# Optimization experiments

Measured on AMD Instinct MI355X. Metric: run time of the kernel, lower is better.

## Reference

```python
import jax, jax.numpy as jnp
import numpy as np

FP8_E4M3_MAX = 448.0
FP4_E2M1_MAX = 6.0
BLOCK = 16  # NVFP4 block-scale granularity


def _round_e4m3(x):
    """Round non-negative values to fp8 e4m3 grid (3 mantissa bits, min normal 2^-6, max 448)."""
    a = jnp.abs(x)
    e = jnp.clip(jnp.floor(jnp.log2(jnp.where(a > 0, a, 1.0))), -6.0, 8.0)
    s = jnp.exp2(e)
    q = jnp.round(a / s * 8.0) / 8.0 * s
    q = jnp.clip(q, 0.0, FP8_E4M3_MAX)
    return jnp.where(a > 0, q, 0.0)


def _round_e2m1(x):
    """Round to fp4 e2m1 grid: +/- {0, 0.5, 1, 1.5, 2, 3, 4, 6}."""
    sgn = jnp.sign(x)
    a = jnp.clip(jnp.abs(x), 0.0, FP4_E2M1_MAX)
    e = jnp.clip(jnp.floor(jnp.log2(jnp.where(a > 0, a, 1.0))), 0.0, 2.0)
    step = jnp.exp2(e) * 0.5  # 0.5 in [0,2), 1 in [2,4), 2 in [4,6]
    q = jnp.round(a / step) * step
    return sgn * jnp.clip(q, 0.0, FP4_E2M1_MAX)


def quant_nvfp4(t):
    """Dynamic NVFP4 quantization (vLLM scaled_fp4_quant semantics).
    Returns (q_fp4 [R, K/16, 16], block_scale_e4m3 [R, K/16], global_scale []).
    Dequant: q * block_scale / global_scale."""
    gs = (FP8_E4M3_MAX * FP4_E2M1_MAX) / jnp.max(jnp.abs(t))
    tb = t.reshape(t.shape[0], -1, BLOCK)
    block_amax = jnp.max(jnp.abs(tb), axis=-1)              # [R, K/16]
    bs = _round_e4m3(block_amax / FP4_E2M1_MAX * gs)         # e4m3 block scales
    safe_bs = jnp.where(bs > 0, bs, 1.0)
    q = _round_e2m1(tb * (gs / safe_bs)[..., None])
    q = jnp.where((bs > 0)[..., None], q, 0.0)
    return q, bs, gs


def setup_inputs() -> dict:
    key = jax.random.key(0)
    kx, kw = jax.random.split(key)
    tokens, hidden = 8192, 4096
    x = jax.random.normal(kx, (tokens, 2 * hidden), dtype=jnp.float32)
    w = jax.random.uniform(kw, (hidden, hidden), dtype=jnp.float32)
    return {"x": x, "w": w}


def reference(x, w):
    d = x.shape[-1] // 2
    # SiluAndMul
    y = jax.nn.silu(x[..., :d]) * x[..., d:]                # [T, H]
    # dynamic NVFP4 quant of activation and weight
    qy, sy, gy = quant_nvfp4(y)
    qw, sw, gw = quant_nvfp4(w)
    # cutlass_scaled_fp4_mm: out = (qy*sy) @ (qw*sw)^T * alpha, alpha = 1/(gy*gw)
    a = (qy * sy[..., None]).reshape(y.shape)               # [T, H]
    b = (qw * sw[..., None]).reshape(w.shape)               # [H, H]
    alpha = 1.0 / (gy * gw)
    return (a @ b.T) * alpha
```

## Files before the change

### kernel.cpp

```cpp
#include <hip/hip_runtime.h>
#include <hip/hip_bf16.h>

typedef __attribute__((ext_vector_type(8))) short bf16x8;
typedef __attribute__((ext_vector_type(4))) float f32x4;
typedef __attribute__((ext_vector_type(16))) float f32x16;


__device__ __forceinline__ float silu_mul_f(float a, float b) {
  float s = 1.0f / (1.0f + expf(-a));
  return (a * s) * b;
}

__device__ __forceinline__ int flog2(float a) {
  return (int)((__float_as_uint(a) >> 23) & 255u) - 127;
}
__device__ __forceinline__ float exp2i(int e) {
  return __uint_as_float((unsigned)(e + 127) << 23);
}

__device__ __forceinline__ float round_e4m3_f(float a) {
  if (!(a > 0.0f)) return 0.0f;
  int e = flog2(a);
  e = e < -6 ? -6 : (e > 8 ? 8 : e);
  float q = rintf(a * exp2i(3 - e)) * exp2i(e - 3);
  return fminf(q, 448.0f);
}

__device__ __forceinline__ float round_e2m1_f(float x) {
  float a = fminf(fabsf(x), 6.0f);
  if (!(a > 0.0f)) return 0.0f;
  int e = flog2(a);
  e = e < 0 ? 0 : (e > 2 ? 2 : e);
  float q = rintf(a * exp2i(1 - e)) * exp2i(e - 1);
  q = fminf(q, 6.0f);
  return (x < 0.0f) ? -q : q;
}

__global__ void init_scal_kernel(float* scal) {
  if (threadIdx.x < 2) scal[threadIdx.x] = 0.0f;
}


__device__ __forceinline__ float act_unit_max(const float* __restrict__ x, long u,
                                              int hidden, long hqm, int hqLog) {
  long row = u >> hqLog, c = u & hqm;
  const float* xr = x + ((row * (long)hidden) << 1);
  float4 v1 = ((const float4*)xr)[c];
  float4 v2 = ((const float4*)(xr + hidden))[c];
  float m = fmaxf(fabsf(silu_mul_f(v1.x, v2.x)), fabsf(silu_mul_f(v1.y, v2.y)));
  m = fmaxf(m, fmaxf(fabsf(silu_mul_f(v1.z, v2.z)), fabsf(silu_mul_f(v1.w, v2.w))));
  return m;
}

__global__ void amax2_kernel(const float* __restrict__ x, const float* __restrict__ w,
                             float* __restrict__ scal, long actU, long wU,
                             int hidden, int hqLog, int AB) {
  const long hqm = (1L << hqLog) - 1;
  float m = 0.0f;
  int which;
  if ((int)blockIdx.x < AB) {
    which = 0;
    const long stride = (long)AB * blockDim.x;
    long u = (long)blockIdx.x * blockDim.x + threadIdx.x;
    for (; u + stride < actU; u += 2 * stride) {
      float m0 = act_unit_max(x, u, hidden, hqm, hqLog);
      float m1 = act_unit_max(x, u + stride, hidden, hqm, hqLog);
      m = fmaxf(m, fmaxf(m0, m1));
    }
    if (u < actU) m = fmaxf(m, act_unit_max(x, u, hidden, hqm, hqLog));
  } else {
    which = 1;
    const long stride = (long)(gridDim.x - AB) * blockDim.x;
    long u = (long)((int)blockIdx.x - AB) * blockDim.x + threadIdx.x;
    for (; u + stride < wU; u += 2 * stride) {
      float4 v1 = ((const float4*)w)[u];
      float4 v2 = ((const float4*)w)[u + stride];
      float m0 = fmaxf(fmaxf(fabsf(v1.x), fabsf(v1.y)), fmaxf(fabsf(v1.z), fabsf(v1.w)));
      float m1 = fmaxf(fmaxf(fabsf(v2.x), fabsf(v2.y)), fmaxf(fabsf(v2.z), fabsf(v2.w)));
      m = fmaxf(m, fmaxf(m0, m1));
    }
    if (u < wU) {
      float4 v = ((const float4*)w)[u];
      m = fmaxf(m, fmaxf(fmaxf(fabsf(v.x), fabsf(v.y)), fmaxf(fabsf(v.z), fabsf(v.w))));
    }
  }
#pragma unroll
  for (int off = 32; off > 0; off >>= 1) m = fmaxf(m, __shfl_xor(m, off));
  __shared__ float sm[4];
  if ((threadIdx.x & 63) == 0) sm[threadIdx.x >> 6] = m;
  __syncthreads();
  if (threadIdx.x == 0) {
    float mm = fmaxf(fmaxf(sm[0], sm[1]), fmaxf(sm[2], sm[3]));
    atomicMax((unsigned int*)(scal + which), __float_as_uint(mm));
  }
}


__device__ __forceinline__ void quant_unit(float y0, float y1, float y2, float y3,
                                           float gs, unsigned short* dst) {
  float lm = fmaxf(fmaxf(fabsf(y0), fabsf(y1)), fmaxf(fabsf(y2), fabsf(y3)));
  lm = fmaxf(lm, __shfl_xor(lm, 1));
  lm = fmaxf(lm, __shfl_xor(lm, 2));
  float bs = round_e4m3_f(lm / 6.0f * gs);
  float r = gs / (bs > 0.0f ? bs : 1.0f);
  ushort4 o;
  o.x = (unsigned short)(__float_as_uint(round_e2m1_f(y0 * r) * bs) >> 16);
  o.y = (unsigned short)(__float_as_uint(round_e2m1_f(y1 * r) * bs) >> 16);
  o.z = (unsigned short)(__float_as_uint(round_e2m1_f(y2 * r) * bs) >> 16);
  o.w = (unsigned short)(__float_as_uint(round_e2m1_f(y3 * r) * bs) >> 16);
  *(ushort4*)dst = o;
}

__global__ void quant2_kernel(const float* __restrict__ x, const float* __restrict__ w,
                              __hip_bfloat16* __restrict__ A, __hip_bfloat16* __restrict__ B,
                              const float* __restrict__ scal, long actU, long wU,
                              int hidden, int hqLog, int AB) {
  const long hqm = (1L << hqLog) - 1;
  if ((int)blockIdx.x < AB) {
    const float gs = 2688.0f / scal[0];
    const long stride = (long)AB * blockDim.x;
    long u = (long)blockIdx.x * blockDim.x + threadIdx.x;
    for (; u + stride < actU; u += 2 * stride) {
      long ua = u, ub = u + stride;
      long ra = ua >> hqLog, ca = ua & hqm;
      long rb = ub >> hqLog, cb = ub & hqm;
      const float* xa = x + ((ra * (long)hidden) << 1) + (ca << 2);
      const float* xb = x + ((rb * (long)hidden) << 1) + (cb << 2);
      float4 a1 = *(const float4*)xa;
      float4 a2 = *(const float4*)(xa + hidden);
      float4 b1 = *(const float4*)xb;
      float4 b2 = *(const float4*)(xb + hidden);
      quant_unit(silu_mul_f(a1.x, a2.x), silu_mul_f(a1.y, a2.y),
                 silu_mul_f(a1.z, a2.z), silu_mul_f(a1.w, a2.w),
                 gs, (unsigned short*)A + (ua << 2));
      quant_unit(silu_mul_f(b1.x, b2.x), silu_mul_f(b1.y, b2.y),
                 silu_mul_f(b1.z, b2.z), silu_mul_f(b1.w, b2.w),
                 gs, (unsigned short*)A + (ub << 2));
    }
    if (u < actU) {
      long c = u & hqm;
      const float* xa = x + (((u >> hqLog) * (long)hidden) << 1) + (c << 2);
      float4 v1 = *(const float4*)xa;
      float4 v2 = *(const float4*)(xa + hidden);
      quant_unit(silu_mul_f(v1.x, v2.x), silu_mul_f(v1.y, v2.y),
                 silu_mul_f(v1.z, v2.z), silu_mul_f(v1.w, v2.w),
                 gs, (unsigned short*)A + (u << 2));
    }
  } else {
    const float gs = 2688.0f / scal[1];
    const long stride = (long)(gridDim.x - AB) * blockDim.x;
    long u = (long)((int)blockIdx.x - AB) * blockDim.x + threadIdx.x;
    for (; u + stride < wU; u += 2 * stride) {
      float4 v1 = ((const float4*)w)[u];
      float4 v2 = ((const float4*)w)[u + stride];
      quant_unit(v1.x, v1.y, v1.z, v1.w, gs, (unsigned short*)B + (u << 2));
      quant_unit(v2.x, v2.y, v2.z, v2.w, gs, (unsigned short*)B + ((u + stride) << 2));
    }
    if (u < wU) {
      float4 v = ((const float4*)w)[u];
      quant_unit(v.x, v.y, v.z, v.w, gs, (unsigned short*)B + (u << 2));
    }
  }
}


__device__ __forceinline__ void gload_lds16(const void* g, void* l) {
  __builtin_amdgcn_global_load_lds(
      (const __attribute__((address_space(1))) void*)(uintptr_t)g,
      (__attribute__((address_space(3))) void*)(uintptr_t)l, 16, 0, 0);
}

template <unsigned IMM>
__device__ __forceinline__ bf16x8 lds_read16o(unsigned addr) {
  bf16x8 r;
  asm volatile("ds_read_b128 %0, %1 offset:%c2" : "=&v"(r) : "v"(addr), "i"(IMM));
  return r;
}

__device__ __forceinline__ f32x16 mfma32(bf16x8 a, bf16x8 b, f32x16 c) {
  return __builtin_amdgcn_mfma_f32_32x32x16_bf16(a, b, c, 0, 0, 0);
}

#define SP1 __builtin_amdgcn_s_setprio(1)
#define SP0 __builtin_amdgcn_s_setprio(0)
#define SCHEDB __builtin_amdgcn_sched_barrier(0)
#define WAITL(n) do { asm volatile("s_waitcnt lgkmcnt(" #n ")" ::: "memory"); SCHEDB; } while (0)
#define VMW4 do { asm volatile("s_waitcnt vmcnt(4)" ::: "memory"); } while (0)

#define STAGEA(PP, HH, KSB) do {                                        \
    const char* _s = pa + (KSB) + (HH) * 64;                            \
    gload_lds16(_s, ldsStA + (PP) * 32768 + (HH) * 16384);              \
    gload_lds16(_s + rowBig, ldsStA + (PP) * 32768 + (HH) * 16384 + 8192); } while (0)

#define STAGEB(PP, HH, KSB) do {                                        \
    const char* _s = pb + (KSB) + (HH) * 64;                            \
    gload_lds16(_s, ldsStB + (PP) * 32768 + (HH) * 16384);              \
    gload_lds16(_s + rowBig, ldsStB + (PP) * 32768 + (HH) * 16384 + 8192); } while (0)

#define RDA(DST, PP, HH, KS) do {                                           \
    DST[0] = lds_read16o<(PP)*32768u + (HH)*16384u + 0u>(vA##KS);           \
    DST[1] = lds_read16o<(PP)*32768u + (HH)*16384u + 2048u>(vA##KS);        \
    DST[2] = lds_read16o<(PP)*32768u + (HH)*16384u + 4096u>(vA##KS);        \
    DST[3] = lds_read16o<(PP)*32768u + (HH)*16384u + 6144u>(vA##KS); } while (0)

#define RDB(DST, PP, HH, KS) do {                                           \
    DST[0] = lds_read16o<(PP)*32768u + (HH)*16384u + 0u>(vB##KS);           \
    DST[1] = lds_read16o<(PP)*32768u + (HH)*16384u + 2048u>(vB##KS); } while (0)

#define MFMA8(AF, BF) do {                               \
    acc[0][0] = mfma32(AF[0], BF[0], acc[0][0]);         \
    acc[1][0] = mfma32(AF[1], BF[0], acc[1][0]);         \
    acc[2][0] = mfma32(AF[2], BF[0], acc[2][0]);         \
    acc[3][0] = mfma32(AF[3], BF[0], acc[3][0]);         \
    acc[0][1] = mfma32(AF[0], BF[1], acc[0][1]);         \
    acc[1][1] = mfma32(AF[1], BF[1], acc[1][1]);         \
    acc[2][1] = mfma32(AF[2], BF[1], acc[2][1]);         \
    acc[3][1] = mfma32(AF[3], BF[1], acc[3][1]); } while (0)

#define TILE(P, KSB) do {                                                \
    STAGEA((P)^1, 0, KSB);                                               \
    RDA(aB, P, 0, 1); RDB(bB, P, 0, 1);                                  \
    WAITL(6);                                                            \
    SP1; MFMA8(aA, bA); SP0;                                             \
    STAGEB((P)^1, 0, KSB);                                               \
    VMW4;                                                                \
    __builtin_amdgcn_s_barrier(); SCHEDB;                                \
    RDA(aA, P, 1, 0); RDB(bA, P, 1, 0);                                  \
    WAITL(6);                                                            \
    SP1; MFMA8(aB, bB); SP0;                                             \
    STAGEA((P)^1, 1, KSB);                                               \
    RDA(aB, P, 1, 1); RDB(bB, P, 1, 1);                                  \
    WAITL(6);                                                            \
    SP1; MFMA8(aA, bA); SP0;                                             \
    STAGEB((P)^1, 1, KSB);                                               \
    VMW4;                                                                \
    __builtin_amdgcn_s_barrier(); SCHEDB;                                \
    RDA(aA, (P)^1, 0, 0); RDB(bA, (P)^1, 0, 0);                          \
    WAITL(6);                                                            \
    SP1; MFMA8(aB, bB); SP0;                                             \
  } while (0)

__global__ __launch_bounds__(512, 2) void gemm_bt_kernel(
    const __hip_bfloat16* __restrict__ A, const __hip_bfloat16* __restrict__ B,
    float* __restrict__ C, const float* __restrict__ scal, int M, int N, int K) {
  __shared__ __align__(16) char lds[131072];

  const int nbm = M >> 8, nbn = N >> 8;
  int wg = blockIdx.x, bm, bn;
  if ((nbm & 7) == 0) {
    int band = nbm >> 3;
    int xcd = wg & 7, c = wg >> 3;
    bm = xcd * band + (c % band);
    bn = c / band;
  } else {
    bm = wg / nbn; bn = wg % nbn;
  }
  const int brow = bm << 8, bcol = bn << 8;

  const int tid = threadIdx.x;
  const int lane = tid & 63;
  const int wave = tid >> 6;
  const int wm = wave >> 2, wn = wave & 3;

  const int srow = tid >> 2;
  const int slc = (tid & 3) ^ ((tid >> 3) & 3);
  const char* pa = (const char*)(A + (size_t)(brow + srow) * K + slc * 8);
  const char* pb = (const char*)(B + (size_t)(bcol + srow) * K + slc * 8);
  const size_t rowBig = (size_t)128 * K * 2;
  char* ldsStA = lds + tid * 16;
  char* ldsStB = lds + 65536 + tid * 16;

  const unsigned ldsBase = (unsigned)(uintptr_t)lds;
  const unsigned l31 = (unsigned)(lane & 31);
  const unsigned half = (unsigned)(lane >> 5);
  const unsigned sw = ((unsigned)lane >> 1) & 3u;
  const unsigned rbyte = l31 * 64u;
  const unsigned vA0 = ldsBase + (unsigned)(wm * 8192) + rbyte + ((half ^ sw) << 4);
  const unsigned vA1 = ldsBase + (unsigned)(wm * 8192) + rbyte + (((2u + half) ^ sw) << 4);
  const unsigned vB0 = ldsBase + 65536u + (unsigned)(wn * 4096) + rbyte + ((half ^ sw) << 4);
  const unsigned vB1 = ldsBase + 65536u + (unsigned)(wn * 4096) + rbyte + (((2u + half) ^ sw) << 4);

  f32x16 acc[4][2] = {};
  bf16x8 aA[4], aB[4], bA[2], bB[2];

  STAGEA(0, 0, 0); STAGEB(0, 0, 0); STAGEA(0, 1, 0); STAGEB(0, 1, 0);
  asm volatile("s_waitcnt vmcnt(0)" ::: "memory");
  __syncthreads();
  RDA(aA, 0, 0, 0); RDB(bA, 0, 0, 0); SCHEDB;

  const int nt = K >> 6;
  for (int it = 0; it < (nt >> 1); ++it) {
    int t0 = it << 1;
    int ks0 = (t0 + 1) * 128;
    int ks1 = (t0 + 2 == nt) ? 0 : (t0 + 2) * 128;
    TILE(0, ks0);
    TILE(1, ks1);
  }
  asm volatile("s_waitcnt lgkmcnt(0)" ::: "memory");
  asm volatile("s_waitcnt vmcnt(0)" ::: "memory");

  float gy = 2688.0f / scal[0];
  float gw = 2688.0f / scal[1];
  float alpha = 1.0f / (gy * gw);

#pragma unroll
  for (int mf = 0; mf < 4; ++mf) {
    int rb = brow + wm * 128 + mf * 32 + (int)(half << 2);
#pragma unroll
    for (int nf = 0; nf < 2; ++nf) {
      int col = bcol + wn * 64 + nf * 32 + (int)l31;
#pragma unroll
      for (int g = 0; g < 4; ++g) {
#pragma unroll
        for (int r = 0; r < 4; ++r) {
          C[(size_t)(rb + 8 * g + r) * N + col] = acc[mf][nf][g * 4 + r] * alpha;
        }
      }
    }
  }
}


extern "C" void kernel_launch(void* const* d_in, const int* in_sizes, int n_in,
                              void* d_out, int out_size, void* d_ws, size_t ws_size,
                              hipStream_t stream) {
  const float* x = (const float*)d_in[0];
  const float* w = (const float*)d_in[1];
  float* out = (float*)d_out;

  int hidden = 1;
  while ((long long)hidden * hidden < (long long)in_sizes[1]) hidden <<= 1;
  int tokens = in_sizes[0] / (2 * hidden);

  char* ws = (char*)d_ws;
  __hip_bfloat16* Aq = (__hip_bfloat16*)ws;
  __hip_bfloat16* Bq = (__hip_bfloat16*)(ws + (size_t)tokens * hidden * 2);
  float* scal = (float*)(ws + (size_t)tokens * hidden * 2 + (size_t)hidden * hidden * 2);

  long actU = (long)tokens * hidden / 4;
  long wU = (long)hidden * hidden / 4;
  int hqLog = __builtin_ctz((unsigned)(hidden >> 2));
  int nBlk = 2048;
  int AB = (int)(((long)nBlk * actU) / (actU + wU));
  AB &= ~3;
  if (AB < 1) AB = 1;
  if (AB > nBlk - 1) AB = nBlk - 1;

  init_scal_kernel<<<1, 64, 0, stream>>>(scal);
  amax2_kernel<<<nBlk, 256, 0, stream>>>(x, w, scal, actU, wU, hidden, hqLog, AB);
  quant2_kernel<<<nBlk, 256, 0, stream>>>(x, w, Aq, Bq, scal, actU, wU, hidden, hqLog, AB);

  int grid = (tokens >> 8) * (hidden >> 8);
  gemm_bt_kernel<<<grid, 512, 0, stream>>>(Aq, Bq, out, scal, tokens, hidden, hidden);
}
```

Before: 395.5 us.

## Switch GEMM inner loop from 32x32x16 to 16x16x32 bf16 MFMA tiles

Replaces the 32x32x16 bf16 MFMA with the 16x16x32 variant, reorganising each wave's 128x64 output tile into 8x4 fragments of 16x16. LDS read addressing, fragment registers and the per-tile interleaving of reads, waits and MFMAs are reworked to match. Each LDS read now covers a full 64-wide K step, so there are fewer k-substeps per tile. The aim is better MFMA throughput or latency hiding. In exchange it issues more MFMA instructions, uses different LDS access patterns and adds a full lgkmcnt(0) wait per tile.

```diff
diff --git a/kernel.cpp b/kernel.cpp
--- a/kernel.cpp
+++ b/kernel.cpp
@@ -3,7 +3,6 @@
 
 typedef __attribute__((ext_vector_type(8))) short bf16x8;
 typedef __attribute__((ext_vector_type(4))) float f32x4;
-typedef __attribute__((ext_vector_type(16))) float f32x16;
 
 
 __device__ __forceinline__ float silu_mul_f(float a, float b) {
@@ -177,8 +176,8 @@
   return r;
 }
 
-__device__ __forceinline__ f32x16 mfma32(bf16x8 a, bf16x8 b, f32x16 c) {
-  return __builtin_amdgcn_mfma_f32_32x32x16_bf16(a, b, c, 0, 0, 0);
+__device__ __forceinline__ f32x4 mfma_(bf16x8 a, bf16x8 b, f32x4 c) {
+  return __builtin_amdgcn_mfma_f32_16x16x32_bf16(a, b, c, 0, 0, 0);
 }
 
 #define SP1 __builtin_amdgcn_s_setprio(1)
@@ -197,47 +196,57 @@
     gload_lds16(_s, ldsStB + (PP) * 32768 + (HH) * 16384);              \
     gload_lds16(_s + rowBig, ldsStB + (PP) * 32768 + (HH) * 16384 + 8192); } while (0)
 
-#define RDA(DST, PP, HH, KS) do {                                           \
-    DST[0] = lds_read16o<(PP)*32768u + (HH)*16384u + 0u>(vA##KS);           \
-    DST[1] = lds_read16o<(PP)*32768u + (HH)*16384u + 2048u>(vA##KS);        \
-    DST[2] = lds_read16o<(PP)*32768u + (HH)*16384u + 4096u>(vA##KS);        \
-    DST[3] = lds_read16o<(PP)*32768u + (HH)*16384u + 6144u>(vA##KS); } while (0)
-
-#define RDB(DST, PP, HH, KS) do {                                           \
-    DST[0] = lds_read16o<(PP)*32768u + (HH)*16384u + 0u>(vB##KS);           \
-    DST[1] = lds_read16o<(PP)*32768u + (HH)*16384u + 2048u>(vB##KS); } while (0)
-
-#define MFMA8(AF, BF) do {                               \
-    acc[0][0] = mfma32(AF[0], BF[0], acc[0][0]);         \
-    acc[1][0] = mfma32(AF[1], BF[0], acc[1][0]);         \
-    acc[2][0] = mfma32(AF[2], BF[0], acc[2][0]);         \
-    acc[3][0] = mfma32(AF[3], BF[0], acc[3][0]);         \
-    acc[0][1] = mfma32(AF[0], BF[1], acc[0][1]);         \
-    acc[1][1] = mfma32(AF[1], BF[1], acc[1][1]);         \
-    acc[2][1] = mfma32(AF[2], BF[1], acc[2][1]);         \
-    acc[3][1] = mfma32(AF[3], BF[1], acc[3][1]); } while (0)
-
-#define TILE(P, KSB) do {                                                \
-    STAGEA((P)^1, 0, KSB);                                               \
-    RDA(aB, P, 0, 1); RDB(bB, P, 0, 1);                                  \
-    WAITL(6);                                                            \
-    SP1; MFMA8(aA, bA); SP0;                                             \
-    STAGEB((P)^1, 0, KSB);                                               \
-    VMW4;                                                                \
-    __builtin_amdgcn_s_barrier(); SCHEDB;                                \
-    RDA(aA, P, 1, 0); RDB(bA, P, 1, 0);                                  \
-    WAITL(6);                                                            \
-    SP1; MFMA8(aB, bB); SP0;                                             \
-    STAGEA((P)^1, 1, KSB);                                               \
-    RDA(aB, P, 1, 1); RDB(bB, P, 1, 1);                                  \
-    WAITL(6);                                                            \
-    SP1; MFMA8(aA, bA); SP0;                                             \
-    STAGEB((P)^1, 1, KSB);                                               \
-    VMW4;                                                                \
-    __builtin_amdgcn_s_barrier(); SCHEDB;                                \
-    RDA(aA, (P)^1, 0, 0); RDB(bA, (P)^1, 0, 0);                          \
-    WAITL(6);                                                            \
-    SP1; MFMA8(aB, bB); SP0;                                             \
+#define RDA4(DST, PP, HH, MB) do {                                              \
+    DST[0] = lds_read16o<(PP)*32768u + (HH)*16384u + ((MB)+0)*1024u>(vA);       \
+    DST[1] = lds_read16o<(PP)*32768u + (HH)*16384u + ((MB)+1)*1024u>(vA);       \
+    DST[2] = lds_read16o<(PP)*32768u + (HH)*16384u + ((MB)+2)*1024u>(vA);       \
+    DST[3] = lds_read16o<(PP)*32768u + (HH)*16384u + ((MB)+3)*1024u>(vA); } while (0)
+
+#define RDB4(DST, PP, HH) do {                                                  \
+    DST[0] = lds_read16o<(PP)*32768u + (HH)*16384u + 0u>(vB);                   \
+    DST[1] = lds_read16o<(PP)*32768u + (HH)*16384u + 1024u>(vB);                \
+    DST[2] = lds_read16o<(PP)*32768u + (HH)*16384u + 2048u>(vB);                \
+    DST[3] = lds_read16o<(PP)*32768u + (HH)*16384u + 3072u>(vB); } while (0)
+
+#define MFMA16(AF, BF, MB) do {                                                  \
+    acc[(MB)+0][0] = mfma_(AF[0], BF[0], acc[(MB)+0][0]);                        \
+    acc[(MB)+1][0] = mfma_(AF[1], BF[0], acc[(MB)+1][0]);                        \
+    acc[(MB)+2][0] = mfma_(AF[2], BF[0], acc[(MB)+2][0]);                        \
+    acc[(MB)+3][0] = mfma_(AF[3], BF[0], acc[(MB)+3][0]);                        \
+    acc[(MB)+0][1] = mfma_(AF[0], BF[1], acc[(MB)+0][1]);                        \
+    acc[(MB)+1][1] = mfma_(AF[1], BF[1], acc[(MB)+1][1]);                        \
+    acc[(MB)+2][1] = mfma_(AF[2], BF[1], acc[(MB)+2][1]);                        \
+    acc[(MB)+3][1] = mfma_(AF[3], BF[1], acc[(MB)+3][1]);                        \
+    acc[(MB)+0][2] = mfma_(AF[0], BF[2], acc[(MB)+0][2]);                        \
+    acc[(MB)+1][2] = mfma_(AF[1], BF[2], acc[(MB)+1][2]);                        \
+    acc[(MB)+2][2] = mfma_(AF[2], BF[2], acc[(MB)+2][2]);                        \
+    acc[(MB)+3][2] = mfma_(AF[3], BF[2], acc[(MB)+3][2]);                        \
+    acc[(MB)+0][3] = mfma_(AF[0], BF[3], acc[(MB)+0][3]);                        \
+    acc[(MB)+1][3] = mfma_(AF[1], BF[3], acc[(MB)+1][3]);                        \
+    acc[(MB)+2][3] = mfma_(AF[2], BF[3], acc[(MB)+2][3]);                        \
+    acc[(MB)+3][3] = mfma_(AF[3], BF[3], acc[(MB)+3][3]); } while (0)
+
+#define TILE(P, KSB) do {                                                        \
+    STAGEA((P)^1, 0, KSB);                                                       \
+    RDA4(aY, P, 0, 4);                                                           \
+    SP1; WAITL(4);                                                               \
+    MFMA16(aX, bb0, 0); SP0;                                                     \
+    STAGEB((P)^1, 0, KSB);                                                       \
+    VMW4;                                                                        \
+    __builtin_amdgcn_s_barrier(); SCHEDB;                                        \
+    RDA4(aX, P, 1, 0); RDB4(bb1, P, 1);                                          \
+    SP1; WAITL(8);                                                               \
+    MFMA16(aY, bb0, 4); SP0;                                                     \
+    STAGEA((P)^1, 1, KSB);                                                       \
+    RDA4(aY, P, 1, 4);                                                           \
+    SP1; WAITL(4);                                                               \
+    MFMA16(aX, bb1, 0); SP0;                                                     \
+    STAGEB((P)^1, 1, KSB);                                                       \
+    WAITL(0);                                                                    \
+    VMW4;                                                                        \
+    __builtin_amdgcn_s_barrier(); SCHEDB;                                        \
+    RDA4(aX, (P)^1, 0, 0); RDB4(bb0, (P)^1, 0); SCHEDB;                          \
+    SP1; MFMA16(aY, bb1, 4); SP0;                                                \
   } while (0)
 
 __global__ __launch_bounds__(512, 2) void gemm_bt_kernel(
@@ -271,22 +280,18 @@
   char* ldsStB = lds + 65536 + tid * 16;
 
   const unsigned ldsBase = (unsigned)(uintptr_t)lds;
-  const unsigned l31 = (unsigned)(lane & 31);
-  const unsigned half = (unsigned)(lane >> 5);
-  const unsigned sw = ((unsigned)lane >> 1) & 3u;
-  const unsigned rbyte = l31 * 64u;
-  const unsigned vA0 = ldsBase + (unsigned)(wm * 8192) + rbyte + ((half ^ sw) << 4);
-  const unsigned vA1 = ldsBase + (unsigned)(wm * 8192) + rbyte + (((2u + half) ^ sw) << 4);
-  const unsigned vB0 = ldsBase + 65536u + (unsigned)(wn * 4096) + rbyte + ((half ^ sw) << 4);
-  const unsigned vB1 = ldsBase + 65536u + (unsigned)(wn * 4096) + rbyte + (((2u + half) ^ sw) << 4);
-
-  f32x16 acc[4][2] = {};
-  bf16x8 aA[4], aB[4], bA[2], bB[2];
+  const unsigned xoff = (unsigned)((lane & 15) * 64) +
+                        ((((unsigned)(lane >> 4)) ^ (((unsigned)lane >> 1) & 3u)) << 4);
+  const unsigned vA = ldsBase + (unsigned)(wm * 8192) + xoff;
+  const unsigned vB = ldsBase + 65536u + (unsigned)(wn * 4096) + xoff;
+
+  f32x4 acc[8][4] = {};
+  bf16x8 aX[4], aY[4], bb0[4], bb1[4];
 
   STAGEA(0, 0, 0); STAGEB(0, 0, 0); STAGEA(0, 1, 0); STAGEB(0, 1, 0);
   asm volatile("s_waitcnt vmcnt(0)" ::: "memory");
   __syncthreads();
-  RDA(aA, 0, 0, 0); RDB(bA, 0, 0, 0); SCHEDB;
+  RDA4(aX, 0, 0, 0); RDB4(bb0, 0, 0); SCHEDB;
 
   const int nt = K >> 6;
   for (int it = 0; it < (nt >> 1); ++it) {
@@ -304,17 +309,14 @@
   float alpha = 1.0f / (gy * gw);
 
 #pragma unroll
-  for (int mf = 0; mf < 4; ++mf) {
-    int rb = brow + wm * 128 + mf * 32 + (int)(half << 2);
+  for (int m = 0; m < 8; ++m) {
+    int rbase = brow + wm * 128 + m * 16 + ((lane >> 4) << 2);
 #pragma unroll
-    for (int nf = 0; nf < 2; ++nf) {
-      int col = bcol + wn * 64 + nf * 32 + (int)l31;
+    for (int n = 0; n < 4; ++n) {
+      int col = bcol + wn * 64 + n * 16 + (lane & 15);
 #pragma unroll
-      for (int g = 0; g < 4; ++g) {
-#pragma unroll
-        for (int r = 0; r < 4; ++r) {
-          C[(size_t)(rb + 8 * g + r) * N + col] = acc[mf][nf][g * 4 + r] * alpha;
-        }
+      for (int rg = 0; rg < 4; ++rg) {
+        C[(size_t)(rbase + rg) * N + col] = acc[m][n][rg] * alpha;
       }
     }
   }
```

New measurement: 387.0 us. -2.2%, faster.
